# Kernel tuning notes

Measured on AMD Instinct MI355X. Metric: run time of the kernel, lower is better.

## Reference

```python
import jax, jax.numpy as jnp
import numpy as np

DIM_IN, DIM_Q, DIM_K, DIM_S, DIM_MLP_S, L, B = 512, 128, 128, 256, 128, 512, 32


def setup_inputs() -> dict:
    key = jax.random.key(0)
    ks = jax.random.split(key, 16)
    s = lambda fan_in: 1.0 / np.sqrt(fan_in)
    inp = {
        "query": jax.random.normal(ks[0], (B, L, DIM_IN), jnp.float32),
        "key": jax.random.normal(ks[1], (B, L, DIM_IN), jnp.float32),
        "value": jax.random.normal(ks[2], (B, L, DIM_IN), jnp.float32),
        "sf": jax.random.normal(ks[3], (B, DIM_S), jnp.float32),
        "atten_mask": jax.random.randint(ks[4], (B, L, L), 0, 2).astype(bool),
        # linear weights stored (in, out); y = x @ W + b
        "Wq": jax.random.normal(ks[5], (DIM_IN, DIM_Q), jnp.float32) * s(DIM_IN),
        "bq": jnp.zeros((DIM_Q,), jnp.float32),
        "Wk": jax.random.normal(ks[6], (DIM_IN, DIM_K), jnp.float32) * s(DIM_IN),
        "bk": jnp.zeros((DIM_K,), jnp.float32),
        "Wv": jax.random.normal(ks[7], (DIM_IN, DIM_K), jnp.float32) * s(DIM_IN),
        "bv": jnp.zeros((DIM_K,), jnp.float32),
        "Wb1": jax.random.normal(ks[8], (DIM_S, DIM_MLP_S), jnp.float32) * s(DIM_S),
        "bb1": jnp.zeros((DIM_MLP_S,), jnp.float32),
        "Wb2": jax.random.normal(ks[9], (DIM_MLP_S, L * L), jnp.float32) * s(DIM_MLP_S),
        "bb2": jnp.zeros((L * L,), jnp.float32),
    }
    return inp


def reference(query, key, value, sf, atten_mask, Wq, bq, Wk, bk, Wv, bv, Wb1, bb1, Wb2, bb2):
    b, l, d = query.shape
    q = query @ Wq + bq          # [b, l, dim_q]
    k = key @ Wk + bk            # [b, l, dim_k]
    v = value @ Wv + bv          # [b, l, dim_k]
    # bias MLP: Linear -> ReLU -> Linear, reshaped to [b, l, l]
    bias = (jax.nn.relu(sf @ Wb1 + bb1) @ Wb2 + bb2).reshape(b, l, l)
    scale = q.shape[-1] ** 0.5
    scores = jnp.einsum("bld,bmd->blm", q, k) / scale
    # faithful to masked_fill_(mask, 1e-9): masked positions become 1e-9, NOT -inf
    scores = jnp.where(atten_mask, jnp.asarray(1e-9, scores.dtype), scores)
    attn = jax.nn.softmax(scores, axis=-1) + bias   # bias added AFTER softmax
    out = jnp.einsum("blm,bmd->bld", attn, v)
    return out
```

## Files before the change

kernel.cpp:

```cpp
#include <hip/hip_runtime.h>


typedef unsigned int   u32;
typedef unsigned short u16;
typedef __attribute__((ext_vector_type(8))) short bf16x8;
typedef __attribute__((ext_vector_type(4))) float f32x4;
typedef __attribute__((ext_vector_type(4))) u32   u32x4;

__device__ __forceinline__ float B2F(u16 x) { return __uint_as_float(((u32)x) << 16); }
__device__ __forceinline__ u16 f2bf(float f) {
    u32 u = __float_as_uint(f);
    return (u16)((u + 0x7fffu + ((u >> 16) & 1u)) >> 16);
}

__global__ __launch_bounds__(256) void mask_detect(const u32* __restrict__ m,
                                                   u32* __restrict__ flag)
{
    const size_t t = (size_t)blockIdx.x * 256 + threadIdx.x;
    u32 any = 0;
#pragma unroll
    for (int l = 0; l < 4; ++l) any |= (m[t * 4 + l] > 1u) ? 1u : 0u;
    if (__ballot(any)) {
        if ((threadIdx.x & 63) == 0) atomicOr(flag, 1u);
    }
}

__global__ __launch_bounds__(256) void mask_canon(const void* __restrict__ mask,
                                                  const u32* __restrict__ flag,
                                                  unsigned char* __restrict__ canon)
{
    const size_t i = (size_t)blockIdx.x * 256 + threadIdx.x;
    if (*flag == 0) canon[i] = (((const int*)mask)[i] != 0) ? 1 : 0;
    else            canon[i] = (((const unsigned char*)mask)[i] != 0) ? 1 : 0;
}

__global__ __launch_bounds__(256) void mask_canon_i32(const int* __restrict__ m,
                                                      unsigned char* __restrict__ canon)
{
    const size_t i = (size_t)blockIdx.x * 256 + threadIdx.x;
    canon[i] = (m[i] != 0) ? 1 : 0;
}

__global__ __launch_bounds__(256) void wtrans(
    const float* __restrict__ Wq, const float* __restrict__ Wk, const float* __restrict__ Wv,
    u16* __restrict__ WT)
{
    const float* W = (blockIdx.y == 0) ? Wq : (blockIdx.y == 1) ? Wk : Wv;
    __shared__ u16 Ts[64][136];
    const int tid = threadIdx.x, kt = blockIdx.x;

    {
        const int kk = tid >> 2, nseg = tid & 3;
        const float4* src = (const float4*)(W + (size_t)(kt * 64 + kk) * 128 + nseg * 32);
#pragma unroll
        for (int j = 0; j < 8; ++j) {
            float4 v = src[j];
            Ts[kk][nseg * 32 + j * 4 + 0] = f2bf(v.x);
            Ts[kk][nseg * 32 + j * 4 + 1] = f2bf(v.y);
            Ts[kk][nseg * 32 + j * 4 + 2] = f2bf(v.z);
            Ts[kk][nseg * 32 + j * 4 + 3] = f2bf(v.w);
        }
    }
    __syncthreads();
    {
        const int n = tid >> 1, kseg = tid & 1;
        u32 pk[16];
#pragma unroll
        for (int j = 0; j < 16; ++j)
            pk[j] = (u32)Ts[kseg * 32 + 2 * j][n] | ((u32)Ts[kseg * 32 + 2 * j + 1][n] << 16);
        u32x4* dst = (u32x4*)(WT + (size_t)blockIdx.y * 65536 + (size_t)n * 512 + kt * 64 + kseg * 32);
        dst[0] = (u32x4){pk[0], pk[1], pk[2], pk[3]};
        dst[1] = (u32x4){pk[4], pk[5], pk[6], pk[7]};
        dst[2] = (u32x4){pk[8], pk[9], pk[10], pk[11]};
        dst[3] = (u32x4){pk[12], pk[13], pk[14], pk[15]};
    }
}

__global__ __launch_bounds__(256) void proj_mfma(
    const float* __restrict__ Xq, const float* __restrict__ Xk, const float* __restrict__ Xv,
    const u16* __restrict__ WT,
    const float* __restrict__ Bq, const float* __restrict__ Bk, const float* __restrict__ Bv,
    u16* __restrict__ Yq, u16* __restrict__ Yk, u16* __restrict__ YvT)
{
    const int s = blockIdx.y;
    const float* X; const float* Bi;
    if (s == 0)      { X = Xq; Bi = Bq; }
    else if (s == 1) { X = Xk; Bi = Bk; }
    else             { X = Xv; Bi = Bv; }
    const u16* Wn = WT + (size_t)s * 65536;

    __shared__ u16 Xs[64][72];
    __shared__ u16 Ws[128][72];

    const int tid  = threadIdx.x;
    const int w    = tid >> 6;
    const int lane = tid & 63;
    const int c    = lane & 15;
    const int qd   = lane >> 4;
    const int R0   = blockIdx.x * 64;

    f32x4 acc[8];
#pragma unroll
    for (int t = 0; t < 8; ++t) acc[t] = (f32x4){0.f, 0.f, 0.f, 0.f};

    for (int kc = 0; kc < 8; ++kc) {
        __syncthreads();
        {
            const int row = tid >> 2, seg = tid & 3;
            const float4* src = (const float4*)(X + (size_t)(R0 + row) * 512 + kc * 64 + seg * 16);
            float4 v0 = src[0], v1 = src[1], v2 = src[2], v3 = src[3];
            u32 pk[8];
            pk[0] = (u32)f2bf(v0.x) | ((u32)f2bf(v0.y) << 16);
            pk[1] = (u32)f2bf(v0.z) | ((u32)f2bf(v0.w) << 16);
            pk[2] = (u32)f2bf(v1.x) | ((u32)f2bf(v1.y) << 16);
            pk[3] = (u32)f2bf(v1.z) | ((u32)f2bf(v1.w) << 16);
            pk[4] = (u32)f2bf(v2.x) | ((u32)f2bf(v2.y) << 16);
            pk[5] = (u32)f2bf(v2.z) | ((u32)f2bf(v2.w) << 16);
            pk[6] = (u32)f2bf(v3.x) | ((u32)f2bf(v3.y) << 16);
            pk[7] = (u32)f2bf(v3.z) | ((u32)f2bf(v3.w) << 16);
            u32x4* dst = (u32x4*)&Xs[row][seg * 16];
            dst[0] = (u32x4){pk[0], pk[1], pk[2], pk[3]};
            dst[1] = (u32x4){pk[4], pk[5], pk[6], pk[7]};
        }
        {
            const int n = tid >> 1, seg = tid & 1;
            const u32x4* src = (const u32x4*)(Wn + (size_t)n * 512 + kc * 64 + seg * 32);
            u32x4 v0 = src[0], v1 = src[1], v2 = src[2], v3 = src[3];
            u32x4* dst = (u32x4*)&Ws[n][seg * 32];
            dst[0] = v0; dst[1] = v1; dst[2] = v2; dst[3] = v3;
        }
        __syncthreads();

#pragma unroll
        for (int ks = 0; ks < 2; ++ks) {
            if (s < 2) {
                const bf16x8 a = *(const bf16x8*)&Xs[w * 16 + c][ks * 32 + qd * 8];
#pragma unroll
                for (int nt = 0; nt < 8; ++nt) {
                    const bf16x8 b = *(const bf16x8*)&Ws[nt * 16 + c][ks * 32 + qd * 8];
                    acc[nt] = __builtin_amdgcn_mfma_f32_16x16x32_bf16(a, b, acc[nt], 0, 0, 0);
                }
            } else {
#pragma unroll
                for (int t = 0; t < 2; ++t) {
                    const bf16x8 a = *(const bf16x8*)&Ws[(2 * w + t) * 16 + c][ks * 32 + qd * 8];
#pragma unroll
                    for (int it = 0; it < 4; ++it) {
                        const bf16x8 b = *(const bf16x8*)&Xs[it * 16 + c][ks * 32 + qd * 8];
                        acc[t * 4 + it] = __builtin_amdgcn_mfma_f32_16x16x32_bf16(a, b, acc[t * 4 + it], 0, 0, 0);
                    }
                }
            }
        }
    }

    if (s < 2) {
        u16* Y = (s == 0) ? Yq : Yk;
#pragma unroll
        for (int nt = 0; nt < 8; ++nt) {
            const float bn = Bi[nt * 16 + c];
#pragma unroll
            for (int r = 0; r < 4; ++r)
                Y[(size_t)(R0 + w * 16 + qd * 4 + r) * 128 + nt * 16 + c] = f2bf(acc[nt][r] + bn);
        }
    } else {
        const int bb = blockIdx.x >> 3, il0 = R0 & 511;
#pragma unroll
        for (int t = 0; t < 2; ++t)
#pragma unroll
            for (int r = 0; r < 4; ++r) {
                const int d = (2 * w + t) * 16 + qd * 4 + r;
                const float bd = Bi[d];
#pragma unroll
                for (int it = 0; it < 4; ++it)
                    YvT[(size_t)bb * 65536 + (size_t)d * 512 + il0 + it * 16 + c] =
                        f2bf(acc[t * 4 + it][r] + bd);
            }
    }
}

__global__ __launch_bounds__(256) void mlp1_kernel(
    const float* __restrict__ sf, const float* __restrict__ Wb1,
    const float* __restrict__ bb1, float* __restrict__ h)
{
    const int t = blockIdx.x * 256 + threadIdx.x;
    const int b = t >> 7, n = t & 127;
    float acc = bb1[n];
    for (int m = 0; m < 256; ++m)
        acc += sf[b * 256 + m] * Wb1[m * 128 + n];
    h[t] = fmaxf(acc, 0.0f);
}

__global__ __launch_bounds__(256) void bias_mlp2(
    const float* __restrict__ h, const float* __restrict__ Wb2,
    const float* __restrict__ bb2, u16* __restrict__ biasb)
{
    __shared__ float hs[4096];
    const int tid = threadIdx.x;
#pragma unroll
    for (int l = 0; l < 16; ++l) hs[l * 256 + tid] = h[l * 256 + tid];
    __syncthreads();

    const size_t n = (size_t)blockIdx.x * 256 + tid;
    float acc[32];
    const float bb = bb2[n];
#pragma unroll
    for (int b = 0; b < 32; ++b) acc[b] = bb;

    for (int m4 = 0; m4 < 32; ++m4) {
        const float w0 = Wb2[(size_t)(m4 * 4 + 0) * 262144 + n];
        const float w1 = Wb2[(size_t)(m4 * 4 + 1) * 262144 + n];
        const float w2 = Wb2[(size_t)(m4 * 4 + 2) * 262144 + n];
        const float w3 = Wb2[(size_t)(m4 * 4 + 3) * 262144 + n];
#pragma unroll
        for (int b = 0; b < 32; ++b) {
            const float4 hv = *(const float4*)&hs[b * 128 + m4 * 4];
            acc[b] += hv.x * w0 + hv.y * w1 + hv.z * w2 + hv.w * w3;
        }
    }
#pragma unroll
    for (int b = 0; b < 32; ++b)
        biasb[(size_t)b * 262144 + n] = f2bf(acc[b]);
}

__global__ __launch_bounds__(512, 2) void attn_mfma8(
    const u16* __restrict__ qb, const u16* __restrict__ kb, const u16* __restrict__ vTb,
    const unsigned char* __restrict__ canon, const u16* __restrict__ biasb,
    float* __restrict__ out)
{
    __shared__ alignas(16) u16 Ks[2][64 * 136];
    __shared__ alignas(16) u16 Ps[2][64 * 72];
    __shared__ alignas(16) u16 Vs[2][128 * 72];
    __shared__ alignas(16) u16 Bs[2][64 * 72];
    __shared__ float redm[2][64];
    __shared__ float reds[2][64];

    const int tid  = threadIdx.x;
    const int g    = tid >> 8;
    const int gtid = tid & 255;
    const int wl   = (tid >> 6) & 3;
    const int lane = tid & 63;
    const int c    = lane & 15;
    const int qd   = lane >> 4;
    const int bb   = blockIdx.x & 31;
    const int it   = blockIdx.x >> 5;
    const int i0   = it * 64;

    bf16x8 qf[4];
    {
        const u16* qp = qb + ((size_t)bb * 512 + i0 + wl * 16 + c) * 128 + qd * 8;
#pragma unroll
        for (int kc = 0; kc < 4; ++kc) qf[kc] = *(const bf16x8*)(qp + kc * 32);
    }

    const int kr_ = gtid >> 2, ksg = gtid & 3;
    const u16* kbase = kb + ((size_t)bb * 512 + g * 256) * 128;
    {
        const u32x4* src = (const u32x4*)(kbase + (size_t)kr_ * 128 + ksg * 32);
        u32x4 k0 = src[0], k1 = src[1], k2 = src[2], k3 = src[3];
        u32x4* dst = (u32x4*)&Ks[g][kr_ * 136 + ksg * 32];
        dst[0] = k0; dst[1] = k1; dst[2] = k2; dst[3] = k3;
    }
    __syncthreads();

    f32x4 S[4][4];
#pragma unroll
    for (int jt = 0; jt < 4; ++jt)
#pragma unroll
        for (int jj = 0; jj < 4; ++jj) S[jt][jj] = (f32x4){0.f, 0.f, 0.f, 0.f};

#pragma unroll
    for (int jt = 0; jt < 4; ++jt) {
        u32x4 k0, k1, k2, k3;
        if (jt < 3) {
            const u32x4* src = (const u32x4*)(kbase + ((size_t)(jt + 1) * 64 + kr_) * 128 + ksg * 32);
            k0 = src[0]; k1 = src[1]; k2 = src[2]; k3 = src[3];
        }
#pragma unroll
        for (int kc = 0; kc < 4; ++kc) {
            const bf16x8 a = qf[kc];
#pragma unroll
            for (int jj = 0; jj < 4; ++jj) {
                const bf16x8 b = *(const bf16x8*)&Ks[g][(jj * 16 + c) * 136 + kc * 32 + qd * 8];
                S[jt][jj] = __builtin_amdgcn_mfma_f32_16x16x32_bf16(a, b, S[jt][jj], 0, 0, 0);
            }
        }
        if (jt < 3) {
            __syncthreads();
            u32x4* dst = (u32x4*)&Ks[g][kr_ * 136 + ksg * 32];
            dst[0] = k0; dst[1] = k1; dst[2] = k2; dst[3] = k3;
            __syncthreads();
        }
    }

    const int vd = gtid >> 1, vsg = gtid & 1;
    const int brw = gtid >> 2, bsg = gtid & 3;
    const u16* vbase = vTb + (size_t)bb * 65536;
    const u16* bbase = biasb + (size_t)bb * 262144;
    u32x4 vr0, vr1, vr2, vr3, br0, br1;
    {
        const u32x4* sv = (const u32x4*)(vbase + (size_t)vd * 512 + (g * 4) * 64 + vsg * 32);
        vr0 = sv[0]; vr1 = sv[1]; vr2 = sv[2]; vr3 = sv[3];
        const u32x4* sb = (const u32x4*)(bbase + (size_t)(i0 + brw) * 512 + (g * 4) * 64 + bsg * 16);
        br0 = sb[0]; br1 = sb[1];
    }

    const float sc = 0.08838834764831845f;
    float lm[4];
#pragma unroll
    for (int r = 0; r < 4; ++r) {
        const int lrow = wl * 16 + qd * 4 + r;
        const unsigned char* cp = canon + ((size_t)bb * 512 + i0 + lrow) * 512 + g * 256;
        float mx = -3.4e38f;
#pragma unroll
        for (int jt = 0; jt < 4; ++jt)
#pragma unroll
            for (int jj = 0; jj < 4; ++jj) {
                float s = S[jt][jj][r] * sc;
                if (cp[jt * 64 + jj * 16 + c]) s = 1e-9f;
                S[jt][jj][r] = s;
                mx = fmaxf(mx, s);
            }
#pragma unroll
        for (int o = 1; o < 16; o <<= 1) mx = fmaxf(mx, __shfl_xor(mx, o, 64));
        lm[r] = mx;
    }
    if (c == 0) {
#pragma unroll
        for (int r = 0; r < 4; ++r) redm[g][wl * 16 + qd * 4 + r] = lm[r];
    }
    __syncthreads();
    float ls[4];
#pragma unroll
    for (int r = 0; r < 4; ++r) {
        const int lrow = wl * 16 + qd * 4 + r;
        const float gmx = fmaxf(redm[0][lrow], redm[1][lrow]);
        float sm = 0.f;
#pragma unroll
        for (int jt = 0; jt < 4; ++jt)
#pragma unroll
            for (int jj = 0; jj < 4; ++jj) {
                const float e = __expf(S[jt][jj][r] - gmx);
                S[jt][jj][r] = e;
                sm += e;
            }
#pragma unroll
        for (int o = 1; o < 16; o <<= 1) sm += __shfl_xor(sm, o, 64);
        ls[r] = sm;
    }
    if (c == 0) {
#pragma unroll
        for (int r = 0; r < 4; ++r) reds[g][wl * 16 + qd * 4 + r] = ls[r];
    }
    __syncthreads();
    float inv_[4];
#pragma unroll
    for (int r = 0; r < 4; ++r) {
        const int lrow = wl * 16 + qd * 4 + r;
        inv_[r] = 1.0f / (reds[0][lrow] + reds[1][lrow]);
    }

    f32x4 O_[8];
#pragma unroll
    for (int ns = 0; ns < 8; ++ns) O_[ns] = (f32x4){0.f, 0.f, 0.f, 0.f};

#pragma unroll
    for (int jt = 0; jt < 4; ++jt) {
        __syncthreads();
        {
            u32x4* dv = (u32x4*)&Vs[g][vd * 72 + vsg * 32];
            dv[0] = vr0; dv[1] = vr1; dv[2] = vr2; dv[3] = vr3;
            u32x4* db = (u32x4*)&Bs[g][brw * 72 + bsg * 16];
            db[0] = br0; db[1] = br1;
        }
        __syncthreads();
        if (jt < 3) {
            const int tg = g * 4 + jt + 1;
            const u32x4* sv = (const u32x4*)(vbase + (size_t)vd * 512 + tg * 64 + vsg * 32);
            vr0 = sv[0]; vr1 = sv[1]; vr2 = sv[2]; vr3 = sv[3];
            const u32x4* sb = (const u32x4*)(bbase + (size_t)(i0 + brw) * 512 + tg * 64 + bsg * 16);
            br0 = sb[0]; br1 = sb[1];
        }
#pragma unroll
        for (int r = 0; r < 4; ++r) {
            const int lrow = wl * 16 + qd * 4 + r;
#pragma unroll
            for (int jj = 0; jj < 4; ++jj) {
                const float p = S[jt][jj][r] * inv_[r] + B2F(Bs[g][lrow * 72 + jj * 16 + c]);
                Ps[g][lrow * 72 + jj * 16 + c] = f2bf(p);
            }
        }
        __syncthreads();
#pragma unroll
        for (int kc = 0; kc < 2; ++kc) {
            const bf16x8 a = *(const bf16x8*)&Ps[g][(wl * 16 + c) * 72 + kc * 32 + qd * 8];
#pragma unroll
            for (int ns = 0; ns < 8; ++ns) {
                const bf16x8 b = *(const bf16x8*)&Vs[g][(ns * 16 + c) * 72 + kc * 32 + qd * 8];
                O_[ns] = __builtin_amdgcn_mfma_f32_16x16x32_bf16(a, b, O_[ns], 0, 0, 0);
            }
        }
    }

    __syncthreads();
    float* Oc = (float*)&Ks[0][0];
    if (g == 1) {
#pragma unroll
        for (int ns = 0; ns < 8; ++ns)
#pragma unroll
            for (int r = 0; r < 4; ++r)
                Oc[(wl * 16 + qd * 4 + r) * 128 + ns * 16 + c] = O_[ns][r];
    }
    __syncthreads();
    if (g == 0) {
#pragma unroll
        for (int ns = 0; ns < 8; ++ns)
#pragma unroll
            for (int r = 0; r < 4; ++r)
                Oc[(wl * 16 + qd * 4 + r) * 128 + ns * 16 + c] += O_[ns][r];
    }
    __syncthreads();
    {
        const int row = tid >> 3, sg = tid & 7;
        const float4* s4 = (const float4*)&Oc[row * 128 + sg * 16];
        float4* d4 = (float4*)(out + ((size_t)bb * 512 + i0 + row) * 128 + sg * 16);
        d4[0] = s4[0]; d4[1] = s4[1]; d4[2] = s4[2]; d4[3] = s4[3];
    }
}

extern "C" void kernel_launch(void* const* d_in, const int* in_sizes, int n_in,
                              void* d_out, int out_size, void* d_ws, size_t ws_size,
                              hipStream_t stream)
{
    const float* query = (const float*)d_in[0];
    const float* key_  = (const float*)d_in[1];
    const float* value = (const float*)d_in[2];
    const float* sf    = (const float*)d_in[3];
    const void*  mask  = d_in[4];
    const float* Wq  = (const float*)d_in[5];
    const float* bq  = (const float*)d_in[6];
    const float* Wk  = (const float*)d_in[7];
    const float* bk  = (const float*)d_in[8];
    const float* Wv  = (const float*)d_in[9];
    const float* bv  = (const float*)d_in[10];
    const float* Wb1 = (const float*)d_in[11];
    const float* bb1 = (const float*)d_in[12];
    const float* Wb2 = (const float*)d_in[13];
    const float* bb2 = (const float*)d_in[14];
    float* out = (float*)d_out;

    char* w = (char*)d_ws;
    u32*   flag     = (u32*)(w);
    unsigned char* canonbuf = (unsigned char*)(w + (1u << 20));
    u16*   qb    = (u16*)(w + (16u << 20));
    u16*   kb    = (u16*)(w + (24u << 20));
    u16*   vTb   = (u16*)(w + (32u << 20));
    float* h     = (float*)(w + (40u << 20));
    u16*   biasb = (u16*)(w + (41u << 20));
    u16*   WT    = (u16*)(w + (58u << 20));

    const unsigned char* canon;
    const bool bytes_conv = (n_in >= 15 && in_sizes[0] == 33554432);
    if (bytes_conv && in_sizes[4] == 8388608) {
        canon = (const unsigned char*)mask;
    } else if (bytes_conv && in_sizes[4] == 33554432) {
        mask_canon_i32<<<32768, 256, 0, stream>>>((const int*)mask, canonbuf);
        canon = canonbuf;
    } else {
        hipMemsetAsync(flag, 0, 4, stream);
        mask_detect<<<2048, 256, 0, stream>>>((const u32*)mask, flag);
        mask_canon<<<32768, 256, 0, stream>>>(mask, flag, canonbuf);
        canon = canonbuf;
    }

    wtrans<<<dim3(8, 3), 256, 0, stream>>>(Wq, Wk, Wv, WT);
    proj_mfma<<<dim3(256, 3), 256, 0, stream>>>(query, key_, value, WT,
                                                bq, bk, bv, qb, kb, vTb);
    mlp1_kernel<<<16, 256, 0, stream>>>(sf, Wb1, bb1, h);
    bias_mlp2<<<1024, 256, 0, stream>>>(h, Wb2, bb2, biasb);
    attn_mfma8<<<256, 512, 0, stream>>>(qb, kb, vTb, canon, biasb, out);
}
```

Baseline: 378.1 us.

## Merge preprocessing kernels into two multi-role launches and restructure bias MLP

The separate mask-detect, weight-transpose and first-MLP kernels are combined into one launch, and the projection GEMM, bias MLP second layer and mask canonicalisation into a second launch that dispatches on block index. This cuts launch count and lets independent work share the GPU at the same time. The bias MLP now has each thread compute two adjacent output columns and read a transposed hidden vector directly from global memory instead of staging it in LDS, which doubles the register accumulators per thread and halves that part's block count.

```diff
diff --git a/kernel.cpp b/kernel.cpp
--- a/kernel.cpp
+++ b/kernel.cpp
@@ -13,214 +13,225 @@
     return (u16)((u + 0x7fffu + ((u >> 16) & 1u)) >> 16);
 }
 
-__global__ __launch_bounds__(256) void mask_detect(const u32* __restrict__ m,
-                                                   u32* __restrict__ flag)
+__global__ __launch_bounds__(256) void prep(
+    const void* __restrict__ mask, u32* __restrict__ flag, int detN,
+    const float* __restrict__ Wq, const float* __restrict__ Wk, const float* __restrict__ Wv,
+    u16* __restrict__ WT,
+    const float* __restrict__ sf, const float* __restrict__ Wb1,
+    const float* __restrict__ bb1, float* __restrict__ hT)
 {
-    const size_t t = (size_t)blockIdx.x * 256 + threadIdx.x;
-    u32 any = 0;
-#pragma unroll
-    for (int l = 0; l < 4; ++l) any |= (m[t * 4 + l] > 1u) ? 1u : 0u;
-    if (__ballot(any)) {
-        if ((threadIdx.x & 63) == 0) atomicOr(flag, 1u);
+    __shared__ u16 Ts[64][136];
+    const int blk = blockIdx.x, tid = threadIdx.x;
+
+    if (blk < detN) {
+        const u32* m = (const u32*)mask;
+        const size_t t = (size_t)blk * 256 + tid;
+        u32 any = 0;
+#pragma unroll
+        for (int l = 0; l < 4; ++l) any |= (m[t * 4 + l] > 1u) ? 1u : 0u;
+        if (__ballot(any)) {
+            if ((tid & 63) == 0) atomicOr(flag, 1u);
+        }
+        return;
+    }
+    if (blk < detN + 24) {
+        const int widx = blk - detN;
+        const int s = widx >> 3, kt = widx & 7;
+        const float* W = (s == 0) ? Wq : (s == 1) ? Wk : Wv;
+        {
+            const int kk = tid >> 2, nseg = tid & 3;
+            const float4* src = (const float4*)(W + (size_t)(kt * 64 + kk) * 128 + nseg * 32);
+#pragma unroll
+            for (int j = 0; j < 8; ++j) {
+                float4 v = src[j];
+                Ts[kk][nseg * 32 + j * 4 + 0] = f2bf(v.x);
+                Ts[kk][nseg * 32 + j * 4 + 1] = f2bf(v.y);
+                Ts[kk][nseg * 32 + j * 4 + 2] = f2bf(v.z);
+                Ts[kk][nseg * 32 + j * 4 + 3] = f2bf(v.w);
+            }
+        }
+        __syncthreads();
+        {
+            const int n = tid >> 1, kseg = tid & 1;
+            u32 pk[16];
+#pragma unroll
+            for (int j = 0; j < 16; ++j)
+                pk[j] = (u32)Ts[kseg * 32 + 2 * j][n] | ((u32)Ts[kseg * 32 + 2 * j + 1][n] << 16);
+            u32x4* dst = (u32x4*)(WT + (size_t)s * 65536 + (size_t)n * 512 + kt * 64 + kseg * 32);
+            dst[0] = (u32x4){pk[0], pk[1], pk[2], pk[3]};
+            dst[1] = (u32x4){pk[4], pk[5], pk[6], pk[7]};
+            dst[2] = (u32x4){pk[8], pk[9], pk[10], pk[11]};
+            dst[3] = (u32x4){pk[12], pk[13], pk[14], pk[15]};
+        }
+        return;
+    }
+    {
+        const int t = (blk - detN - 24) * 256 + tid;
+        const int b = t >> 7, n = t & 127;
+        float acc = bb1[n];
+        for (int m = 0; m < 256; ++m)
+            acc += sf[b * 256 + m] * Wb1[m * 128 + n];
+        hT[n * 32 + b] = fmaxf(acc, 0.0f);
     }
 }
 
-__global__ __launch_bounds__(256) void mask_canon(const void* __restrict__ mask,
-                                                  const u32* __restrict__ flag,
-                                                  unsigned char* __restrict__ canon)
-{
-    const size_t i = (size_t)blockIdx.x * 256 + threadIdx.x;
-    if (*flag == 0) canon[i] = (((const int*)mask)[i] != 0) ? 1 : 0;
-    else            canon[i] = (((const unsigned char*)mask)[i] != 0) ? 1 : 0;
-}
-
-__global__ __launch_bounds__(256) void mask_canon_i32(const int* __restrict__ m,
-                                                      unsigned char* __restrict__ canon)
-{
-    const size_t i = (size_t)blockIdx.x * 256 + threadIdx.x;
-    canon[i] = (m[i] != 0) ? 1 : 0;
-}
-
-__global__ __launch_bounds__(256) void wtrans(
-    const float* __restrict__ Wq, const float* __restrict__ Wk, const float* __restrict__ Wv,
-    u16* __restrict__ WT)
-{
-    const float* W = (blockIdx.y == 0) ? Wq : (blockIdx.y == 1) ? Wk : Wv;
-    __shared__ u16 Ts[64][136];
-    const int tid = threadIdx.x, kt = blockIdx.x;
-
-    {
-        const int kk = tid >> 2, nseg = tid & 3;
-        const float4* src = (const float4*)(W + (size_t)(kt * 64 + kk) * 128 + nseg * 32);
-#pragma unroll
-        for (int j = 0; j < 8; ++j) {
-            float4 v = src[j];
-            Ts[kk][nseg * 32 + j * 4 + 0] = f2bf(v.x);
-            Ts[kk][nseg * 32 + j * 4 + 1] = f2bf(v.y);
-            Ts[kk][nseg * 32 + j * 4 + 2] = f2bf(v.z);
-            Ts[kk][nseg * 32 + j * 4 + 3] = f2bf(v.w);
-        }
-    }
-    __syncthreads();
-    {
-        const int n = tid >> 1, kseg = tid & 1;
-        u32 pk[16];
-#pragma unroll
-        for (int j = 0; j < 16; ++j)
-            pk[j] = (u32)Ts[kseg * 32 + 2 * j][n] | ((u32)Ts[kseg * 32 + 2 * j + 1][n] << 16);
-        u32x4* dst = (u32x4*)(WT + (size_t)blockIdx.y * 65536 + (size_t)n * 512 + kt * 64 + kseg * 32);
-        dst[0] = (u32x4){pk[0], pk[1], pk[2], pk[3]};
-        dst[1] = (u32x4){pk[4], pk[5], pk[6], pk[7]};
-        dst[2] = (u32x4){pk[8], pk[9], pk[10], pk[11]};
-        dst[3] = (u32x4){pk[12], pk[13], pk[14], pk[15]};
-    }
-}
-
-__global__ __launch_bounds__(256) void proj_mfma(
+__global__ __launch_bounds__(256) void mid(
     const float* __restrict__ Xq, const float* __restrict__ Xk, const float* __restrict__ Xv,
     const u16* __restrict__ WT,
     const float* __restrict__ Bq, const float* __restrict__ Bk, const float* __restrict__ Bv,
-    u16* __restrict__ Yq, u16* __restrict__ Yk, u16* __restrict__ YvT)
+    u16* __restrict__ Yq, u16* __restrict__ Yk, u16* __restrict__ YvT,
+    const float* __restrict__ hT, const float* __restrict__ Wb2,
+    const float* __restrict__ bb2, u16* __restrict__ biasb,
+    const void* __restrict__ mask, const u32* __restrict__ flag, int mode,
+    unsigned char* __restrict__ canonbuf)
 {
-    const int s = blockIdx.y;
-    const float* X; const float* Bi;
-    if (s == 0)      { X = Xq; Bi = Bq; }
-    else if (s == 1) { X = Xk; Bi = Bk; }
-    else             { X = Xv; Bi = Bv; }
-    const u16* Wn = WT + (size_t)s * 65536;
-
     __shared__ u16 Xs[64][72];
     __shared__ u16 Ws[128][72];
-
-    const int tid  = threadIdx.x;
-    const int w    = tid >> 6;
-    const int lane = tid & 63;
-    const int c    = lane & 15;
-    const int qd   = lane >> 4;
-    const int R0   = blockIdx.x * 64;
-
-    f32x4 acc[8];
-#pragma unroll
-    for (int t = 0; t < 8; ++t) acc[t] = (f32x4){0.f, 0.f, 0.f, 0.f};
-
-    for (int kc = 0; kc < 8; ++kc) {
-        __syncthreads();
+    const int blk = blockIdx.x, tid = threadIdx.x;
+
+    if (blk < 512) {
+        const size_t n0 = ((size_t)blk * 256 + tid) * 2;
+        float ax[32], ay[32];
         {
-            const int row = tid >> 2, seg = tid & 3;
-            const float4* src = (const float4*)(X + (size_t)(R0 + row) * 512 + kc * 64 + seg * 16);
-            float4 v0 = src[0], v1 = src[1], v2 = src[2], v3 = src[3];
-            u32 pk[8];
-            pk[0] = (u32)f2bf(v0.x) | ((u32)f2bf(v0.y) << 16);
-            pk[1] = (u32)f2bf(v0.z) | ((u32)f2bf(v0.w) << 16);
-            pk[2] = (u32)f2bf(v1.x) | ((u32)f2bf(v1.y) << 16);
-            pk[3] = (u32)f2bf(v1.z) | ((u32)f2bf(v1.w) << 16);
-            pk[4] = (u32)f2bf(v2.x) | ((u32)f2bf(v2.y) << 16);
-            pk[5] = (u32)f2bf(v2.z) | ((u32)f2bf(v2.w) << 16);
-            pk[6] = (u32)f2bf(v3.x) | ((u32)f2bf(v3.y) << 16);
-            pk[7] = (u32)f2bf(v3.z) | ((u32)f2bf(v3.w) << 16);
-            u32x4* dst = (u32x4*)&Xs[row][seg * 16];
-            dst[0] = (u32x4){pk[0], pk[1], pk[2], pk[3]};
-            dst[1] = (u32x4){pk[4], pk[5], pk[6], pk[7]};
-        }
-        {
-            const int n = tid >> 1, seg = tid & 1;
-            const u32x4* src = (const u32x4*)(Wn + (size_t)n * 512 + kc * 64 + seg * 32);
-            u32x4 v0 = src[0], v1 = src[1], v2 = src[2], v3 = src[3];
-            u32x4* dst = (u32x4*)&Ws[n][seg * 32];
-            dst[0] = v0; dst[1] = v1; dst[2] = v2; dst[3] = v3;
-        }
-        __syncthreads();
-
-#pragma unroll
-        for (int ks = 0; ks < 2; ++ks) {
-            if (s < 2) {
-                const bf16x8 a = *(const bf16x8*)&Xs[w * 16 + c][ks * 32 + qd * 8];
-#pragma unroll
-                for (int nt = 0; nt < 8; ++nt) {
-                    const bf16x8 b = *(const bf16x8*)&Ws[nt * 16 + c][ks * 32 + qd * 8];
-                    acc[nt] = __builtin_amdgcn_mfma_f32_16x16x32_bf16(a, b, acc[nt], 0, 0, 0);
-                }
-            } else {
-#pragma unroll
-                for (int t = 0; t < 2; ++t) {
-                    const bf16x8 a = *(const bf16x8*)&Ws[(2 * w + t) * 16 + c][ks * 32 + qd * 8];
-#pragma unroll
-                    for (int it = 0; it < 4; ++it) {
-                        const bf16x8 b = *(const bf16x8*)&Xs[it * 16 + c][ks * 32 + qd * 8];
-                        acc[t * 4 + it] = __builtin_amdgcn_mfma_f32_16x16x32_bf16(a, b, acc[t * 4 + it], 0, 0, 0);
+            const float2 bb = *(const float2*)&bb2[n0];
+#pragma unroll
+            for (int b = 0; b < 32; ++b) { ax[b] = bb.x; ay[b] = bb.y; }
+        }
+#pragma unroll 2
+        for (int m = 0; m < 128; ++m) {
+            const float2 w2 = *(const float2*)&Wb2[(size_t)m * 262144 + n0];
+            const float* hrow = hT + m * 32;
+#pragma unroll
+            for (int b = 0; b < 32; ++b) {
+                const float hv = hrow[b];
+                ax[b] += w2.x * hv;
+                ay[b] += w2.y * hv;
+            }
+        }
+#pragma unroll
+        for (int b = 0; b < 32; ++b) {
+            const u32 pk = (u32)f2bf(ax[b]) | ((u32)f2bf(ay[b]) << 16);
+            *(u32*)(biasb + (size_t)b * 262144 + n0) = pk;
+        }
+        return;
+    }
+
+    if (blk < 1280) {
+        const int pidx = blk - 512;
+        const int s = pidx >> 8;
+        const int R0 = (pidx & 255) * 64;
+        const float* X; const float* Bi;
+        if (s == 0)      { X = Xq; Bi = Bq; }
+        else if (s == 1) { X = Xk; Bi = Bk; }
+        else             { X = Xv; Bi = Bv; }
+        const u16* Wn = WT + (size_t)s * 65536;
+
+        const int w    = tid >> 6;
+        const int lane = tid & 63;
+        const int c    = lane & 15;
+        const int qd   = lane >> 4;
+
+        f32x4 acc[8];
+#pragma unroll
+        for (int t = 0; t < 8; ++t) acc[t] = (f32x4){0.f, 0.f, 0.f, 0.f};
+
+        for (int kc = 0; kc < 8; ++kc) {
+            __syncthreads();
+            {
+                const int row = tid >> 2, seg = tid & 3;
+                const float4* src = (const float4*)(X + (size_t)(R0 + row) * 512 + kc * 64 + seg * 16);
+                float4 v0 = src[0], v1 = src[1], v2 = src[2], v3 = src[3];
+                u32 pk[8];
+                pk[0] = (u32)f2bf(v0.x) | ((u32)f2bf(v0.y) << 16);
+                pk[1] = (u32)f2bf(v0.z) | ((u32)f2bf(v0.w) << 16);
+                pk[2] = (u32)f2bf(v1.x) | ((u32)f2bf(v1.y) << 16);
+                pk[3] = (u32)f2bf(v1.z) | ((u32)f2bf(v1.w) << 16);
+                pk[4] = (u32)f2bf(v2.x) | ((u32)f2bf(v2.y) << 16);
+                pk[5] = (u32)f2bf(v2.z) | ((u32)f2bf(v2.w) << 16);
+                pk[6] = (u32)f2bf(v3.x) | ((u32)f2bf(v3.y) << 16);
+                pk[7] = (u32)f2bf(v3.z) | ((u32)f2bf(v3.w) << 16);
+                u32x4* dst = (u32x4*)&Xs[row][seg * 16];
+                dst[0] = (u32x4){pk[0], pk[1], pk[2], pk[3]};
+                dst[1] = (u32x4){pk[4], pk[5], pk[6], pk[7]};
+            }
+            {
+                const int n = tid >> 1, seg = tid & 1;
+                const u32x4* src = (const u32x4*)(Wn + (size_t)n * 512 + kc * 64 + seg * 32);
+                u32x4 v0 = src[0], v1 = src[1], v2 = src[2], v3 = src[3];
+                u32x4* dst = (u32x4*)&Ws[n][seg * 32];
+                dst[0] = v0; dst[1] = v1; dst[2] = v2; dst[3] = v3;
+            }
+            __syncthreads();
+
+#pragma unroll
+            for (int ks = 0; ks < 2; ++ks) {
+                if (s < 2) {
+                    const bf16x8 a = *(const bf16x8*)&Xs[w * 16 + c][ks * 32 + qd * 8];
+#pragma unroll
+                    for (int nt = 0; nt < 8; ++nt) {
+                        const bf16x8 b = *(const bf16x8*)&Ws[nt * 16 + c][ks * 32 + qd * 8];
+                        acc[nt] = __builtin_amdgcn_mfma_f32_16x16x32_bf16(a, b, acc[nt], 0, 0, 0);
+                    }
+                } else {
+#pragma unroll
+                    for (int t = 0; t < 2; ++t) {
+                        const bf16x8 a = *(const bf16x8*)&Ws[(2 * w + t) * 16 + c][ks * 32 + qd * 8];
+#pragma unroll
+                        for (int it = 0; it < 4; ++it) {
+                            const bf16x8 b = *(const bf16x8*)&Xs[it * 16 + c][ks * 32 + qd * 8];
+                            acc[t * 4 + it] = __builtin_amdgcn_mfma_f32_16x16x32_bf16(a, b, acc[t * 4 + it], 0, 0, 0);
+                        }
                     }
                 }
             }
         }
-    }
-
-    if (s < 2) {
-        u16* Y = (s == 0) ? Yq : Yk;
-#pragma unroll
-        for (int nt = 0; nt < 8; ++nt) {
-            const float bn = Bi[nt * 16 + c];
-#pragma unroll
-            for (int r = 0; r < 4; ++r)
-                Y[(size_t)(R0 + w * 16 + qd * 4 + r) * 128 + nt * 16 + c] = f2bf(acc[nt][r] + bn);
-        }
-    } else {
-        const int bb = blockIdx.x >> 3, il0 = R0 & 511;
-#pragma unroll
-        for (int t = 0; t < 2; ++t)
-#pragma unroll
-            for (int r = 0; r < 4; ++r) {
-                const int d = (2 * w + t) * 16 + qd * 4 + r;
-                const float bd = Bi[d];
-#pragma unroll
-                for (int it = 0; it < 4; ++it)
-                    YvT[(size_t)bb * 65536 + (size_t)d * 512 + il0 + it * 16 + c] =
-                        f2bf(acc[t * 4 + it][r] + bd);
-            }
-    }
-}
-
-__global__ __launch_bounds__(256) void mlp1_kernel(
-    const float* __restrict__ sf, const float* __restrict__ Wb1,
-    const float* __restrict__ bb1, float* __restrict__ h)
-{
-    const int t = blockIdx.x * 256 + threadIdx.x;
-    const int b = t >> 7, n = t & 127;
-    float acc = bb1[n];
-    for (int m = 0; m < 256; ++m)
-        acc += sf[b * 256 + m] * Wb1[m * 128 + n];
-    h[t] = fmaxf(acc, 0.0f);
-}
-
-__global__ __launch_bounds__(256) void bias_mlp2(
-    const float* __restrict__ h, const float* __restrict__ Wb2,
-    const float* __restrict__ bb2, u16* __restrict__ biasb)
-{
-    __shared__ float hs[4096];
-    const int tid = threadIdx.x;
-#pragma unroll
-    for (int l = 0; l < 16; ++l) hs[l * 256 + tid] = h[l * 256 + tid];
-    __syncthreads();
-
-    const size_t n = (size_t)blockIdx.x * 256 + tid;
-    float acc[32];
-    const float bb = bb2[n];
-#pragma unroll
-    for (int b = 0; b < 32; ++b) acc[b] = bb;
-
-    for (int m4 = 0; m4 < 32; ++m4) {
-        const float w0 = Wb2[(size_t)(m4 * 4 + 0) * 262144 + n];
-        const float w1 = Wb2[(size_t)(m4 * 4 + 1) * 262144 + n];
-        const float w2 = Wb2[(size_t)(m4 * 4 + 2) * 262144 + n];
-        const float w3 = Wb2[(size_t)(m4 * 4 + 3) * 262144 + n];
-#pragma unroll
-        for (int b = 0; b < 32; ++b) {
-            const float4 hv = *(const float4*)&hs[b * 128 + m4 * 4];
-            acc[b] += hv.x * w0 + hv.y * w1 + hv.z * w2 + hv.w * w3;
-        }
-    }
-#pragma unroll
-    for (int b = 0; b < 32; ++b)
-        biasb[(size_t)b * 262144 + n] = f2bf(acc[b]);
+
+        if (s < 2) {
+            u16* Y = (s == 0) ? Yq : Yk;
+#pragma unroll
+            for (int nt = 0; nt < 8; ++nt) {
+                const float bn = Bi[nt * 16 + c];
+#pragma unroll
+                for (int r = 0; r < 4; ++r)
+                    Y[(size_t)(R0 + w * 16 + qd * 4 + r) * 128 + nt * 16 + c] = f2bf(acc[nt][r] + bn);
+            }
+        } else {
+            const int bb = (pidx & 255) >> 3, il0 = R0 & 511;
+#pragma unroll
+            for (int t = 0; t < 2; ++t)
+#pragma unroll
+                for (int r = 0; r < 4; ++r) {
+                    const int d = (2 * w + t) * 16 + qd * 4 + r;
+                    const float bd = Bi[d];
+#pragma unroll
+                    for (int it = 0; it < 4; ++it)
+                        YvT[(size_t)bb * 65536 + (size_t)d * 512 + il0 + it * 16 + c] =
+                            f2bf(acc[t * 4 + it][r] + bd);
+                }
+        }
+        return;
+    }
+
+    {
+        const int cb = blk - 1280;
+        const size_t base = (size_t)cb * 4096;
+        const bool i32src = (mode == 2) || (mode == 0 && *flag == 0);
+        if (i32src) {
+            const int* mi = (const int*)mask;
+#pragma unroll
+            for (int j = 0; j < 16; ++j) {
+                const size_t i = base + (size_t)j * 256 + tid;
+                canonbuf[i] = mi[i] ? 1 : 0;
+            }
+        } else {
+            const unsigned char* mb = (const unsigned char*)mask;
+#pragma unroll
+            for (int j = 0; j < 16; ++j) {
+                const size_t i = base + (size_t)j * 256 + tid;
+                canonbuf[i] = mb[i] ? 1 : 0;
+            }
+        }
+    }
 }
 
 __global__ __launch_bounds__(512, 2) void attn_mfma8(
@@ -455,28 +466,27 @@
     u16*   qb    = (u16*)(w + (16u << 20));
     u16*   kb    = (u16*)(w + (24u << 20));
     u16*   vTb   = (u16*)(w + (32u << 20));
-    float* h     = (float*)(w + (40u << 20));
+    float* hT    = (float*)(w + (40u << 20));
     u16*   biasb = (u16*)(w + (41u << 20));
     u16*   WT    = (u16*)(w + (58u << 20));
 
-    const unsigned char* canon;
-    const bool bytes_conv = (n_in >= 15 && in_sizes[0] == 33554432);
-    if (bytes_conv && in_sizes[4] == 8388608) {
-        canon = (const unsigned char*)mask;
-    } else if (bytes_conv && in_sizes[4] == 33554432) {
-        mask_canon_i32<<<32768, 256, 0, stream>>>((const int*)mask, canonbuf);
-        canon = canonbuf;
-    } else {
-        hipMemsetAsync(flag, 0, 4, stream);
-        mask_detect<<<2048, 256, 0, stream>>>((const u32*)mask, flag);
-        mask_canon<<<32768, 256, 0, stream>>>(mask, flag, canonbuf);
-        canon = canonbuf;
-    }
-
-    wtrans<<<dim3(8, 3), 256, 0, stream>>>(Wq, Wk, Wv, WT);
-    proj_mfma<<<dim3(256, 3), 256, 0, stream>>>(query, key_, value, WT,
-                                                bq, bk, bv, qb, kb, vTb);
-    mlp1_kernel<<<16, 256, 0, stream>>>(sf, Wb1, bb1, h);
-    bias_mlp2<<<1024, 256, 0, stream>>>(h, Wb2, bb2, biasb);
+    int mode = 0;
+    if (n_in >= 15 && in_sizes[0] == 33554432) {
+        if (in_sizes[4] == 8388608)       mode = 1;
+        else if (in_sizes[4] == 33554432) mode = 2;
+    }
+    if (mode == 0) hipMemsetAsync(flag, 0, 4, stream);
+
+    const int detN = (mode == 0) ? 2048 : 0;
+    prep<<<detN + 40, 256, 0, stream>>>(mask, flag, detN, Wq, Wk, Wv, WT,
+                                        sf, Wb1, bb1, hT);
+
+    const int canN = (mode != 1) ? 2048 : 0;
+    mid<<<1280 + canN, 256, 0, stream>>>(query, key_, value, WT,
+                                         bq, bk, bv, qb, kb, vTb,
+                                         hT, Wb2, bb2, biasb,
+                                         mask, flag, mode, canonbuf);
+
+    const unsigned char* canon = (mode == 1) ? (const unsigned char*)mask : canonbuf;
     attn_mfma8<<<256, 512, 0, stream>>>(qb, kb, vTb, canon, biasb, out);
 }
```

After: 345.2 us. 8.7% less time.
